# Performance work log

Hardware: AMD Instinct MI355X
Metric: run time of the kernel (lower is better)

## Reference

```python
import jax, jax.numpy as jnp
import numpy as np

D_MODEL = 512
N = 1024
BS = 64


def setup_inputs() -> dict:
    key = jax.random.key(0)
    ks = jax.random.split(key, 4)
    x = jax.random.normal(ks[0], (BS, N, D_MODEL), dtype=jnp.float32)
    # nn.Linear init per init_weights(): weight ~ N(0, 0.001), bias = 0
    Wq = 0.001 * jax.random.normal(ks[1], (D_MODEL, D_MODEL), dtype=jnp.float32)
    Wk = 0.001 * jax.random.normal(ks[2], (D_MODEL, D_MODEL), dtype=jnp.float32)
    Wv = 0.001 * jax.random.normal(ks[3], (D_MODEL, D_MODEL), dtype=jnp.float32)
    bq = jnp.zeros((D_MODEL,), dtype=jnp.float32)
    bk = jnp.zeros((D_MODEL,), dtype=jnp.float32)
    bv = jnp.zeros((D_MODEL,), dtype=jnp.float32)
    pos_bias = jnp.ones((N, N), dtype=jnp.float32)  # nn.Parameter(ones)
    return {"x": x, "Wq": Wq, "bq": bq, "Wk": Wk, "bk": bk,
            "Wv": Wv, "bv": bv, "pos_bias": pos_bias}


def reference(x, Wq, bq, Wk, bk, Wv, bv, pos_bias):
    # q,k,v: [bs, n, d] via Linear (y = x W^T + b)
    q = jnp.einsum('bnd,ed->bne', x, Wq) + bq
    k = jnp.einsum('bnd,ed->bne', x, Wk) + bk
    v = jnp.einsum('bnd,ed->bne', x, Wv) + bv
    # exp(k[b,j,d] + bias[i,j]) factorizes exactly: exp(bias) * exp(k).
    # This avoids the (n, bs, n, d) broadcast intermediate of the original
    # while computing identical math.
    ek = jnp.exp(k)                                   # [bs, n, d]
    eb = jnp.exp(pos_bias)                            # [n_i, n_j]
    numerator = jnp.einsum('ij,bjd->bid', eb, ek * v)  # sum over j
    denominator = jnp.einsum('ij,bjd->bid', eb, ek)
    out = jax.nn.sigmoid(q) * (numerator / denominator)  # [bs, n, d]
    return out
```

## Files before the change

### kernel.cpp

```cpp
#include <hip/hip_runtime.h>
#include <hip/hip_bf16.h>
#include <stdint.h>


#define NSEQ 1024
#define DM   512

typedef __attribute__((ext_vector_type(8))) short bf16x8;
typedef __attribute__((ext_vector_type(4))) float f32x4;

static __device__ __forceinline__ float b2f(unsigned short u) {
    union { uint32_t i; float f; } c; c.i = ((uint32_t)u) << 16; return c.f;
}
static __device__ __forceinline__ unsigned short f2b(float f) {
    union { float f; uint32_t i; } c; c.f = f;
    uint32_t r = c.i + 0x7FFFu + ((c.i >> 16) & 1u);
    return (unsigned short)(r >> 16);
}
static __device__ __forceinline__ void gl_lds16(const unsigned short* g, unsigned short* l) {
    __builtin_amdgcn_global_load_lds(
        (const __attribute__((address_space(1))) unsigned int*)(g),
        (__attribute__((address_space(3))) unsigned int*)(l), 16, 0, 0);
}

#define PH_BAR() do { asm volatile("" ::: "memory"); \
    __builtin_amdgcn_s_barrier(); asm volatile("" ::: "memory"); } while (0)

__global__ void k_flag0(unsigned int* flag) { *flag = 0u; }

__global__ void k_flag(const float* __restrict__ pb, unsigned int* __restrict__ flag) {
    int i = blockIdx.x * 256 + threadIdx.x;
    float4 v = reinterpret_cast<const float4*>(pb)[i];
    float p0 = pb[0];
    if (v.x != p0 || v.y != p0 || v.z != p0 || v.w != p0) atomicOr(flag, 1u);
}

__global__ void k_eb(const float* __restrict__ pb, unsigned short* __restrict__ eb,
                     const unsigned int* __restrict__ flag) {
    if (*flag == 0u) return;
    int i = blockIdx.x * 256 + threadIdx.x;
    float4 v = reinterpret_cast<const float4*>(pb)[i];
    union { unsigned short u[4]; uint2 p; } o;
    o.u[0] = f2b(__expf(v.x)); o.u[1] = f2b(__expf(v.y));
    o.u[2] = f2b(__expf(v.z)); o.u[3] = f2b(__expf(v.w));
    reinterpret_cast<uint2*>(eb)[i] = o.p;
}

__global__ void k_cvt(const float* __restrict__ src, unsigned short* __restrict__ dst) {
    int i = blockIdx.x * 256 + threadIdx.x;
    const float4* p = reinterpret_cast<const float4*>(src) + (size_t)i * 2;
    float4 f0 = p[0], f1 = p[1];
    union { unsigned short u[8]; int4 v; } o;
    o.u[0]=f2b(f0.x); o.u[1]=f2b(f0.y); o.u[2]=f2b(f0.z); o.u[3]=f2b(f0.w);
    o.u[4]=f2b(f1.x); o.u[5]=f2b(f1.y); o.u[6]=f2b(f1.z); o.u[7]=f2b(f1.w);
    reinterpret_cast<int4*>(dst)[i] = o.v;
}

__global__ void k_cvt_kv(const float* __restrict__ src, unsigned short* __restrict__ Wb,
                         int toff) {
    int i = blockIdx.x * 256 + threadIdx.x;
    int r = i >> 6, c8 = i & 63;
    const float4* p = reinterpret_cast<const float4*>(src + (size_t)r * DM + c8 * 8);
    float4 f0 = p[0], f1 = p[1];
    union { unsigned short u[8]; int4 v; } o;
    o.u[0]=f2b(f0.x); o.u[1]=f2b(f0.y); o.u[2]=f2b(f0.z); o.u[3]=f2b(f0.w);
    o.u[4]=f2b(f1.x); o.u[5]=f2b(f1.y); o.u[6]=f2b(f1.z); o.u[7]=f2b(f1.w);
    int r2 = 512 + ((r >> 7) << 8) + ((r & 127) << 1) + toff;
    *reinterpret_cast<int4*>(&Wb[(size_t)r2 * DM + c8 * 8]) = o.v;
}

template<int NT>
static __device__ __forceinline__ void gemm_p(
    const unsigned short* __restrict__ Abase,
    const unsigned short* __restrict__ Bbase,
    int lda, int ldb, unsigned short* smem, f32x4 (&acc)[8][4],
    int wave, int lane)
{
    const int wr = wave >> 2, wq = wave & 3;
    const int lrow = lane & 15, lkg = lane >> 4;
    const int po  = lane >> 3;
    const int sub = (lane >> 2) & 1;
    const int qp  = lane & 3;

    auto stage = [&](int mat, int s, int h, int t) {
        int p = h * 64 + wave * 8 + po;
        int r = p * 2 + sub;
        int q = qp ^ (p & 3);
        int col = ((t & (NT - 1)) << 5) + q * 8;
        const unsigned short* g = (mat ? Bbase + (size_t)r * ldb
                                       : Abase + (size_t)r * lda) + col;
        unsigned short* d = smem + mat * 32768 + s * 8192 + (h * 64 + wave * 8) * 64;
        gl_lds16(g, d);
    };
    auto loadA = [&](int s, int h, bf16x8* af) {
        const unsigned short* base = smem + s * 8192;
        #pragma unroll
        for (int mi = 0; mi < 4; ++mi) {
            int r = wr * 128 + h * 64 + mi * 16 + lrow;
            int p = r >> 1;
            af[mi] = *reinterpret_cast<const bf16x8*>(
                base + p * 64 + (r & 1) * 32 + ((lkg ^ (p & 3)) << 3));
        }
    };
    auto loadB = [&](int s, bf16x8* bf) {
        const unsigned short* base = smem + 32768 + s * 8192;
        #pragma unroll
        for (int ni = 0; ni < 4; ++ni) {
            int r = wq * 64 + ni * 16 + lrow;
            int p = r >> 1;
            bf[ni] = *reinterpret_cast<const bf16x8*>(
                base + p * 64 + (r & 1) * 32 + ((lkg ^ (p & 3)) << 3));
        }
    };
    auto mfma16 = [&](int h, bf16x8* af, bf16x8* bf) {
        __builtin_amdgcn_s_setprio(1);
        #pragma unroll
        for (int mi = 0; mi < 4; ++mi)
            #pragma unroll
            for (int ni = 0; ni < 4; ++ni)
                acc[h * 4 + mi][ni] = __builtin_amdgcn_mfma_f32_16x16x32_bf16(
                    af[mi], bf[ni], acc[h * 4 + mi][ni], 0, 0, 0);
        __builtin_amdgcn_s_setprio(0);
    };

    #pragma unroll
    for (int pt = 0; pt < 3; ++pt) {
        stage(0, pt, 0, pt); stage(0, pt, 1, pt);
        stage(1, pt, 0, pt); stage(1, pt, 1, pt);
    }
    asm volatile("s_waitcnt vmcnt(8)" ::: "memory");
    __builtin_amdgcn_s_barrier();

    #pragma unroll 1
    for (int tt = 0; tt < NT; tt += 4) {
        #pragma unroll
        for (int u = 0; u < 4; ++u) {
            const int t = tt + u;
            const int s = u, s3 = (u + 3) & 3, t3 = t + 3;
            bf16x8 af[4], bfr[4];
            loadB(s, bfr); loadA(s, 0, af);
            stage(0, s3, 0, t3); stage(0, s3, 1, t3);
            mfma16(0, af, bfr);
            loadA(s, 1, af);
            stage(1, s3, 0, t3); stage(1, s3, 1, t3);
            mfma16(1, af, bfr);
            asm volatile("s_waitcnt vmcnt(8)" ::: "memory");
            __builtin_amdgcn_s_barrier();
        }
    }
    asm volatile("s_waitcnt vmcnt(0)" ::: "memory");
    __builtin_amdgcn_s_barrier();
}

__launch_bounds__(512)
__global__ void k_kv(const unsigned short* __restrict__ xb,
                     const unsigned short* __restrict__ Wb,
                     const float* __restrict__ bk, const float* __restrict__ bv,
                     unsigned short* __restrict__ Z,
                     float* __restrict__ P,
                     const unsigned int* __restrict__ flag)
{
    extern __shared__ unsigned short smem[];
    const int bid = blockIdx.x;
    const int logical = (bid & 7) * 128 + (bid >> 3);
    const int mtile = logical >> 2, e4 = logical & 3;
    const int brow = mtile * 256;
    const int b = brow >> 10, jtile = (brow >> 8) & 3;
    const bool uni = (*flag == 0u);

    const int tid = threadIdx.x;
    const int lane = tid & 63, wave = tid >> 6;
    const int wr = wave >> 2, wq = wave & 3;
    const int lrow = lane & 15, lkg = lane >> 4;

    f32x4 acc[8][4];
    const f32x4 z4 = {0.f, 0.f, 0.f, 0.f};
    #pragma unroll
    for (int a = 0; a < 8; ++a)
        #pragma unroll
        for (int c = 0; c < 4; ++c) acc[a][c] = z4;

    gemm_p<16>(xb + (size_t)brow * DM, Wb + (size_t)(512 + e4 * 256) * DM, DM, DM,
               smem, acc, wave, lane);

    if (uni) {
        const int sub = lrow & 1;
        float* SF = reinterpret_cast<float*>(smem);
        float se[4], sv2[4];
        #pragma unroll
        for (int ni = 0; ni < 4; ++ni) {
            int n = wq * 64 + ni * 16 + lrow;
            int d = e4 * 128 + (n >> 1);
            float bia = sub ? bv[d] : bk[d];
            float accv = 0.f, acce = 0.f;
            #pragma unroll
            for (int mi = 0; mi < 8; ++mi) {
                #pragma unroll
                for (int r = 0; r < 4; ++r) {
                    float val = acc[mi][ni][r] + bia;
                    float e = sub ? val : __expf(val);
                    float partner = __shfl_xor(e, 1);
                    if (!sub) { accv += e * partner; acce += e; }
                }
            }
            accv += __shfl_xor(accv, 16); accv += __shfl_xor(accv, 32);
            acce += __shfl_xor(acce, 16); acce += __shfl_xor(acce, 32);
            se[ni] = acce; sv2[ni] = accv;
        }
        __syncthreads();
        if (sub == 0 && lkg == 0) {
            #pragma unroll
            for (int ni = 0; ni < 4; ++ni) {
                int dl = wq * 32 + ni * 8 + (lrow >> 1);
                SF[wr * 256 + dl * 2]     = sv2[ni];
                SF[wr * 256 + dl * 2 + 1] = se[ni];
            }
        }
        __syncthreads();
        if (tid < 128) {
            int dl = tid, d = e4 * 128 + dl;
            float num = SF[dl * 2]     + SF[256 + dl * 2];
            float den = SF[dl * 2 + 1] + SF[256 + dl * 2 + 1];
            P[b * 2048 + jtile * 512 + d] = num;
            P[131072 + b * 2048 + jtile * 512 + d] = den;
        }
    } else {
        unsigned short* T = smem;
        #pragma unroll
        for (int pp = 0; pp < 2; ++pp) {
            __syncthreads();
            if (wr == pp) {
                #pragma unroll
                for (int mi = 0; mi < 8; ++mi) {
                    int m0 = mi*16 + lkg*4;
                    #pragma unroll
                    for (int ni = 0; ni < 4; ++ni) {
                        int n = wq*64 + ni*16 + lrow;
                        int sub = n & 1;
                        int d = e4 * 128 + (n >> 1);
                        float bia = sub ? bv[d] : bk[d];
                        union { unsigned short u[4]; uint2 p; } o;
                        #pragma unroll
                        for (int r = 0; r < 4; ++r) {
                            float tv = acc[mi][ni][r] + bia;
                            o.u[r] = f2b(sub ? tv : __expf(tv));
                        }
                        *reinterpret_cast<uint2*>(&T[n * 136 + m0]) = o.p;
                    }
                }
            }
            __syncthreads();
            const int j0 = (brow & (NSEQ - 1)) + pp * 128;
            #pragma unroll
            for (int it = 0; it < 8; ++it) {
                int idx = it * 512 + tid;
                int zr = idx >> 4, jg = idx & 15;
                int t = zr >> 7, dli = zr & 127;
                int d = e4 * 128 + dli;
                union { unsigned short u[8]; int4 v; } o;
                if (t == 0) {
                    union { unsigned short u[8]; int4 v; } pe, pv;
                    pe.v = *reinterpret_cast<const int4*>(&T[(2*dli)     * 136 + jg*8]);
                    pv.v = *reinterpret_cast<const int4*>(&T[(2*dli + 1) * 136 + jg*8]);
                    #pragma unroll
                    for (int j = 0; j < 8; ++j) o.u[j] = f2b(b2f(pe.u[j]) * b2f(pv.u[j]));
                } else {
                    o.v = *reinterpret_cast<const int4*>(&T[(2*dli) * 136 + jg*8]);
                }
                int nz = ((d >> 4) << 5) + t * 16 + (d & 15);
                size_t off = ((size_t)(b * NSEQ + nz)) * NSEQ + j0 + jg * 8;
                *reinterpret_cast<int4*>(&Z[off]) = o.v;
            }
        }
    }
}

__launch_bounds__(256)
__global__ void k_sum2(const float* __restrict__ P,
                       const unsigned int* __restrict__ flag,
                       float* __restrict__ R)
{
    if (*flag != 0u) return;
    int gid = blockIdx.x * 256 + threadIdx.x;
    int b = gid >> 9, d = gid & 511;
    const float* p0 = P + b * 2048 + d;
    const float* p1 = P + 131072 + b * 2048 + d;
    float num = p0[0] + p0[512] + p0[1024] + p0[1536];
    float den = p1[0] + p1[512] + p1[1024] + p1[1536];
    R[gid] = num / den;
}

__launch_bounds__(512)
__global__ void k_q(const unsigned short* __restrict__ xb,
                    const unsigned short* __restrict__ Wb,
                    const float* __restrict__ bq,
                    const float* __restrict__ R,
                    unsigned short* __restrict__ s_out,
                    float* __restrict__ out,
                    const unsigned int* __restrict__ flag)
{
    extern __shared__ unsigned short smem[];
    const int bid = blockIdx.x;
    const int logical = (bid & 7) * 64 + (bid >> 3);
    const int mtile = logical >> 1, etile = logical & 1;
    const int brow = mtile * 256;
    const int ecol = etile * 256;
    const int b = brow >> 10;
    const bool uni = (*flag == 0u);

    const int tid = threadIdx.x;
    const int lane = tid & 63, wave = tid >> 6;
    const int wr = wave >> 2, wq = wave & 3;
    const int lrow = lane & 15, lkg = lane >> 4;

    f32x4 acc[8][4];
    const f32x4 z4 = {0.f, 0.f, 0.f, 0.f};
    #pragma unroll
    for (int a = 0; a < 8; ++a)
        #pragma unroll
        for (int c = 0; c < 4; ++c) acc[a][c] = z4;

    gemm_p<16>(xb + (size_t)brow * DM, Wb + (size_t)ecol * DM, DM, DM,
               smem, acc, wave, lane);

    unsigned short* T = smem;
    #pragma unroll
    for (int pp = 0; pp < 2; ++pp) {
        __syncthreads();
        if ((wq >> 1) == pp) {
            #pragma unroll
            for (int mi = 0; mi < 8; ++mi) {
                int m0 = wr*128 + mi*16 + lkg*4;
                #pragma unroll
                for (int ni = 0; ni < 4; ++ni) {
                    int nl = (wq & 1) * 64 + ni*16 + lrow;
                    float bia = bq[ecol + pp*128 + nl];
                    #pragma unroll
                    for (int r = 0; r < 4; ++r) {
                        float tq = acc[mi][ni][r] + bia;
                        float sg = __builtin_amdgcn_rcpf(1.f + __expf(-tq));
                        T[(m0 + r) * 136 + nl] = f2b(sg);
                    }
                }
            }
        }
        __syncthreads();
        if (uni) {
            #pragma unroll
            for (int it = 0; it < 8; ++it) {
                int idx = it * 512 + tid;
                int m = idx >> 4, ng = idx & 15;
                union { unsigned short u[8]; int4 v; } sv;
                sv.v = *reinterpret_cast<const int4*>(&T[m * 136 + ng * 8]);
                int dcol = ecol + pp * 128 + ng * 8;
                const float4* rp = reinterpret_cast<const float4*>(&R[b * 512 + dcol]);
                float4 r0 = rp[0], r1 = rp[1];
                float4 o0, o1;
                o0.x = b2f(sv.u[0]) * r0.x; o0.y = b2f(sv.u[1]) * r0.y;
                o0.z = b2f(sv.u[2]) * r0.z; o0.w = b2f(sv.u[3]) * r0.w;
                o1.x = b2f(sv.u[4]) * r1.x; o1.y = b2f(sv.u[5]) * r1.y;
                o1.z = b2f(sv.u[6]) * r1.z; o1.w = b2f(sv.u[7]) * r1.w;
                float4* op = reinterpret_cast<float4*>(
                    &out[(size_t)(brow + m) * DM + dcol]);
                op[0] = o0; op[1] = o1;
            }
        } else {
            #pragma unroll
            for (int it = 0; it < 8; ++it) {
                int idx = it * 512 + tid;
                int m = idx >> 4, ng = idx & 15;
                int4 vv = *reinterpret_cast<const int4*>(&T[m * 136 + ng * 8]);
                *reinterpret_cast<int4*>(
                    &s_out[(size_t)(brow + m) * DM + ecol + pp*128 + ng * 8]) = vv;
            }
        }
    }
}

__launch_bounds__(512)
__global__ void k_aft(const unsigned short* __restrict__ eb,
                      const unsigned short* __restrict__ Z,
                      const unsigned short* __restrict__ s_in,
                      const unsigned int* __restrict__ flag,
                      float* __restrict__ out)
{
    if (*flag == 0u) return;
    extern __shared__ unsigned short smem[];
    const int bid = blockIdx.x;
    const int logical = (bid & 7) * 32 + (bid >> 3);
    const int itile = logical & 3, ncol = logical >> 2;
    const int i0 = itile * 256;

    const int tid = threadIdx.x;
    const int lane = tid & 63, wave = tid >> 6;
    const int wr = wave >> 2, wq = wave & 3;
    const int lrow = lane & 15, lkg = lane >> 4;
    const int po = lane >> 3, sub = (lane >> 2) & 1, qp = lane & 3;
    const int ch0 = wave * 2;

    const unsigned short* Abase = eb + (size_t)i0 * NSEQ;
    const unsigned short* Bbase = Z + (size_t)ncol * 4 * 256 * NSEQ;

    f32x4 acc[8][4];
    const f32x4 z4 = {0.f, 0.f, 0.f, 0.f};
    #pragma unroll
    for (int a = 0; a < 8; ++a)
        #pragma unroll
        for (int c = 0; c < 4; ++c) acc[a][c] = z4;

    auto half = [&](int isB, int d, int c) -> unsigned short* {
        return smem + isB * 32768 + (d * 2 + c) * 8192;
    };
    auto stg = [&](int isB, int d, int c, int t) {
        int ta = t & 63, gp = ta >> 4, tk = ta & 15;
        unsigned short* dst = half(isB, d, c);
        #pragma unroll
        for (int q2 = 0; q2 < 2; ++q2) {
            int ch = ch0 + q2;
            int p = ch * 8 + po, r = p * 2 + sub;
            int col = (tk << 6) + (c << 5) + ((qp ^ (p & 3)) << 3);
            const unsigned short* g = isB
                ? Bbase + ((size_t)(gp * 256 + r)) * NSEQ + col
                : Abase + (size_t)r * NSEQ + col;
            gl_lds16(g, dst + ch * 512);
        }
    };
    auto ldA = [&](int d, int c, int h, bf16x8* af) {
        const unsigned short* base = half(0, d, c);
        #pragma unroll
        for (int mi = 0; mi < 4; ++mi) {
            int r = wr * 128 + h * 64 + mi * 16 + lrow, p = r >> 1;
            af[mi] = *reinterpret_cast<const bf16x8*>(
                base + p * 64 + (r & 1) * 32 + ((lkg ^ (p & 3)) << 3));
        }
    };
    auto ldB = [&](int d, int c, bf16x8* bf) {
        const unsigned short* base = half(1, d, c);
        #pragma unroll
        for (int ni = 0; ni < 4; ++ni) {
            int r = wq * 64 + ni * 16 + lrow, p = r >> 1;
            bf[ni] = *reinterpret_cast<const bf16x8*>(
                base + p * 64 + (r & 1) * 32 + ((lkg ^ (p & 3)) << 3));
        }
    };
    auto mm = [&](int h, bf16x8* af, bf16x8* bf) {
        __builtin_amdgcn_s_setprio(1);
        #pragma unroll
        for (int mi = 0; mi < 4; ++mi)
            #pragma unroll
            for (int ni = 0; ni < 4; ++ni)
                acc[h * 4 + mi][ni] = __builtin_amdgcn_mfma_f32_16x16x32_bf16(
                    af[mi], bf[ni], acc[h * 4 + mi][ni], 0, 0, 0);
        __builtin_amdgcn_s_setprio(0);
    };

    stg(0, 0, 0, 0); stg(1, 0, 0, 0);
    stg(0, 0, 1, 0); stg(1, 0, 1, 0);
    stg(0, 1, 0, 1); stg(1, 1, 0, 1);
    asm volatile("s_waitcnt vmcnt(4)" ::: "memory");
    __builtin_amdgcn_s_barrier();
    asm volatile("" ::: "memory");

    #pragma unroll 1
    for (int g = 0; g < 4; ++g) {
        #pragma unroll 1
        for (int ii = 0; ii < 8; ++ii) {
            const int T = (g << 4) + (ii << 1);
            const int U = T + 1, T2 = T + 2, U2 = T + 3;
            bf16x8 af[4], bf[4];
            ldB(0, 0, bf); ldA(0, 0, 0, af); stg(0, 1, 1, U);
            PH_BAR(); mm(0, af, bf); PH_BAR();
            ldA(0, 0, 1, af); stg(1, 1, 1, U);
            PH_BAR(); mm(1, af, bf); PH_BAR();
            ldB(0, 1, bf); ldA(0, 1, 0, af); stg(0, 0, 0, T2);
            PH_BAR(); mm(0, af, bf); PH_BAR();
            ldA(0, 1, 1, af); stg(1, 0, 0, T2);
            asm volatile("s_waitcnt vmcnt(4)" ::: "memory");
            PH_BAR(); mm(1, af, bf); PH_BAR();
            ldB(1, 0, bf); ldA(1, 0, 0, af); stg(0, 0, 1, T2);
            PH_BAR(); mm(0, af, bf); PH_BAR();
            ldA(1, 0, 1, af); stg(1, 0, 1, T2);
            PH_BAR(); mm(1, af, bf); PH_BAR();
            ldB(1, 1, bf); ldA(1, 1, 0, af); stg(0, 1, 0, U2);
            PH_BAR(); mm(0, af, bf); PH_BAR();
            ldA(1, 1, 1, af); stg(1, 1, 0, U2);
            asm volatile("s_waitcnt vmcnt(4)" ::: "memory");
            PH_BAR(); mm(1, af, bf); PH_BAR();
        }
        const int n0 = (ncol * 4 + g) * 256;
        #pragma unroll
        for (int mi = 0; mi < 8; ++mi) {
            int i = i0 + wr*128 + mi*16 + lkg*4;
            #pragma unroll
            for (int pi = 0; pi < 2; ++pi) {
                int nA = n0 + wq*64 + pi*32 + lrow;
                int b  = nA >> 10, nn = nA & (NSEQ - 1);
                int d  = ((nn >> 5) << 4) + (nn & 15);
                #pragma unroll
                for (int r = 0; r < 4; ++r) {
                    size_t o = ((size_t)(b * NSEQ + i + r)) * DM + d;
                    out[o] = b2f(s_in[o]) * acc[mi][pi*2][r] / acc[mi][pi*2 + 1][r];
                }
                acc[mi][pi*2] = z4; acc[mi][pi*2 + 1] = z4;
            }
        }
    }
    asm volatile("s_waitcnt vmcnt(0)" ::: "memory");
}

extern "C" void kernel_launch(void* const* d_in, const int* in_sizes, int n_in,
                              void* d_out, int out_size, void* d_ws, size_t ws_size,
                              hipStream_t stream)
{
    const float* x  = (const float*)d_in[0];
    const float* Wq = (const float*)d_in[1];
    const float* bq = (const float*)d_in[2];
    const float* Wk = (const float*)d_in[3];
    const float* bk = (const float*)d_in[4];
    const float* Wv = (const float*)d_in[5];
    const float* bv = (const float*)d_in[6];
    const float* pb = (const float*)d_in[7];
    float* out = (float*)d_out;

    char* ws = (char*)d_ws;
    unsigned short* eb   = (unsigned short*)(ws);
    float*          Pbuf = (float*)(ws);
    unsigned short* Wb   = (unsigned short*)(ws + ((size_t)2 << 20));
    unsigned int*   flag = (unsigned int*)(ws + 0x380000);
    float*          Rbuf = (float*)(ws + 0x384000);
    unsigned short* xb   = (unsigned short*)(ws + ((size_t)4   << 20));
    unsigned short* s    = (unsigned short*)(ws + ((size_t)68  << 20));
    unsigned short* Z    = (unsigned short*)(ws + ((size_t)132 << 20));

    k_flag0<<<1, 1, 0, stream>>>(flag);
    k_flag<<<1024, 256, 0, stream>>>(pb, flag);
    k_eb <<<1024, 256, 0, stream>>>(pb, eb, flag);
    k_cvt<<<16384, 256, 0, stream>>>(x,  xb);
    k_cvt<<<128,   256, 0, stream>>>(Wq, Wb);
    k_cvt_kv<<<128, 256, 0, stream>>>(Wk, Wb, 0);
    k_cvt_kv<<<128, 256, 0, stream>>>(Wv, Wb, 1);
    k_kv<<<1024, 512, 131072, stream>>>(xb, Wb, bk, bv, Z, Pbuf, flag);
    k_sum2<<<128, 256, 0, stream>>>(Pbuf, flag, Rbuf);
    k_q<<<512, 512, 131072, stream>>>(xb, Wb, bq, Rbuf, s, out, flag);
    k_aft<<<256, 512, 131072, stream>>>(eb, Z, s, flag, out);
}
```

Before: 212.8 us.

## Shrink k_q tiles to 128x128 with inline double-buffered LDS GEMM loop

Rewrites the Q projection kernel to use 128x128 output tiles instead of 256x256. It replaces the shared gemm_p helper with an inline double-buffered global-to-LDS pipeline using swizzled addressing. Shared memory drops to about 34KB and the grid grows to 2048 blocks, which should raise occupancy and improve load balance across CUs. The cost is less data reuse per block, so more global and L2 traffic is spent on re-reading x and W. It also changes the sub-lane selector in k_kv from lrow&1 to lane&1; since lane&15 and lane keep the same low bit, this is equivalent.

```diff
diff --git a/kernel.cpp b/kernel.cpp
--- a/kernel.cpp
+++ b/kernel.cpp
@@ -184,7 +184,7 @@
                smem, acc, wave, lane);
 
     if (uni) {
-        const int sub = lrow & 1;
+        const int sub = lane & 1;
         float* SF = reinterpret_cast<float*>(smem);
         float se[4], sv2[4];
         #pragma unroll
@@ -301,10 +301,10 @@
 {
     extern __shared__ unsigned short smem[];
     const int bid = blockIdx.x;
-    const int logical = (bid & 7) * 64 + (bid >> 3);
-    const int mtile = logical >> 1, etile = logical & 1;
-    const int brow = mtile * 256;
-    const int ecol = etile * 256;
+    const int logical = (bid & 7) * 256 + (bid >> 3);
+    const int mtile = logical >> 2, etile = logical & 3;
+    const int brow = mtile * 128;
+    const int ecol = etile * 128;
     const int b = brow >> 10;
     const bool uni = (*flag == 0u);
 
@@ -312,67 +312,115 @@
     const int lane = tid & 63, wave = tid >> 6;
     const int wr = wave >> 2, wq = wave & 3;
     const int lrow = lane & 15, lkg = lane >> 4;
-
-    f32x4 acc[8][4];
+    const int po = lane >> 3, sub = (lane >> 2) & 1, qp = lane & 3;
+
+    const unsigned short* Abase = xb + (size_t)brow * DM;
+    const unsigned short* Bbase = Wb + (size_t)ecol * DM;
+
+    f32x4 acc[4][2];
     const f32x4 z4 = {0.f, 0.f, 0.f, 0.f};
     #pragma unroll
-    for (int a = 0; a < 8; ++a)
-        #pragma unroll
-        for (int c = 0; c < 4; ++c) acc[a][c] = z4;
-
-    gemm_p<16>(xb + (size_t)brow * DM, Wb + (size_t)ecol * DM, DM, DM,
-               smem, acc, wave, lane);
+    for (int a = 0; a < 4; ++a)
+        #pragma unroll
+        for (int c = 0; c < 2; ++c) acc[a][c] = z4;
+
+    auto stg = [&](int mat, int s, int t) {
+        int p = wave * 8 + po;
+        int r = p * 2 + sub;
+        int q = qp ^ (p & 3);
+        int col = (t << 5) + q * 8;
+        const unsigned short* g = (mat ? Bbase + (size_t)r * DM
+                                       : Abase + (size_t)r * DM) + col;
+        gl_lds16(g, smem + mat * 8192 + s * 4096 + (wave * 8) * 64);
+    };
+    auto ldA = [&](int s, bf16x8* af) {
+        const unsigned short* base = smem + s * 4096;
+        #pragma unroll
+        for (int mi = 0; mi < 4; ++mi) {
+            int r = wr * 64 + mi * 16 + lrow, p = r >> 1;
+            af[mi] = *reinterpret_cast<const bf16x8*>(
+                base + p * 64 + (r & 1) * 32 + ((lkg ^ (p & 3)) << 3));
+        }
+    };
+    auto ldB = [&](int s, bf16x8* bf) {
+        const unsigned short* base = smem + 8192 + s * 4096;
+        #pragma unroll
+        for (int ni = 0; ni < 2; ++ni) {
+            int r = wq * 32 + ni * 16 + lrow, p = r >> 1;
+            bf[ni] = *reinterpret_cast<const bf16x8*>(
+                base + p * 64 + (r & 1) * 32 + ((lkg ^ (p & 3)) << 3));
+        }
+    };
+
+    stg(0, 0, 0); stg(1, 0, 0);
+    asm volatile("s_waitcnt vmcnt(0)" ::: "memory");
+    __builtin_amdgcn_s_barrier();
+
+    #pragma unroll 1
+    for (int tt = 0; tt < 16; tt += 2) {
+        #pragma unroll
+        for (int u = 0; u < 2; ++u) {
+            const int t = tt + u;
+            const int s = u, sn = u ^ 1;
+            if (t + 1 < 16) { stg(0, sn, t + 1); stg(1, sn, t + 1); }
+            bf16x8 af[4], bf[2];
+            ldB(s, bf); ldA(s, af);
+            __builtin_amdgcn_s_setprio(1);
+            #pragma unroll
+            for (int mi = 0; mi < 4; ++mi)
+                #pragma unroll
+                for (int ni = 0; ni < 2; ++ni)
+                    acc[mi][ni] = __builtin_amdgcn_mfma_f32_16x16x32_bf16(
+                        af[mi], bf[ni], acc[mi][ni], 0, 0, 0);
+            __builtin_amdgcn_s_setprio(0);
+            asm volatile("s_waitcnt vmcnt(0)" ::: "memory");
+            __builtin_amdgcn_s_barrier();
+        }
+    }
 
     unsigned short* T = smem;
     #pragma unroll
-    for (int pp = 0; pp < 2; ++pp) {
-        __syncthreads();
-        if ((wq >> 1) == pp) {
-            #pragma unroll
-            for (int mi = 0; mi < 8; ++mi) {
-                int m0 = wr*128 + mi*16 + lkg*4;
-                #pragma unroll
-                for (int ni = 0; ni < 4; ++ni) {
-                    int nl = (wq & 1) * 64 + ni*16 + lrow;
-                    float bia = bq[ecol + pp*128 + nl];
-                    #pragma unroll
-                    for (int r = 0; r < 4; ++r) {
-                        float tq = acc[mi][ni][r] + bia;
-                        float sg = __builtin_amdgcn_rcpf(1.f + __expf(-tq));
-                        T[(m0 + r) * 136 + nl] = f2b(sg);
-                    }
-                }
+    for (int mi = 0; mi < 4; ++mi) {
+        int m0 = wr * 64 + mi * 16 + lkg * 4;
+        #pragma unroll
+        for (int ni = 0; ni < 2; ++ni) {
+            int nl = wq * 32 + ni * 16 + lrow;
+            float bia = bq[ecol + nl];
+            #pragma unroll
+            for (int r = 0; r < 4; ++r) {
+                float tq = acc[mi][ni][r] + bia;
+                float sg = __builtin_amdgcn_rcpf(1.f + __expf(-tq));
+                T[(m0 + r) * 136 + nl] = f2b(sg);
             }
         }
-        __syncthreads();
-        if (uni) {
-            #pragma unroll
-            for (int it = 0; it < 8; ++it) {
-                int idx = it * 512 + tid;
-                int m = idx >> 4, ng = idx & 15;
-                union { unsigned short u[8]; int4 v; } sv;
-                sv.v = *reinterpret_cast<const int4*>(&T[m * 136 + ng * 8]);
-                int dcol = ecol + pp * 128 + ng * 8;
-                const float4* rp = reinterpret_cast<const float4*>(&R[b * 512 + dcol]);
-                float4 r0 = rp[0], r1 = rp[1];
-                float4 o0, o1;
-                o0.x = b2f(sv.u[0]) * r0.x; o0.y = b2f(sv.u[1]) * r0.y;
-                o0.z = b2f(sv.u[2]) * r0.z; o0.w = b2f(sv.u[3]) * r0.w;
-                o1.x = b2f(sv.u[4]) * r1.x; o1.y = b2f(sv.u[5]) * r1.y;
-                o1.z = b2f(sv.u[6]) * r1.z; o1.w = b2f(sv.u[7]) * r1.w;
-                float4* op = reinterpret_cast<float4*>(
-                    &out[(size_t)(brow + m) * DM + dcol]);
-                op[0] = o0; op[1] = o1;
-            }
-        } else {
-            #pragma unroll
-            for (int it = 0; it < 8; ++it) {
-                int idx = it * 512 + tid;
-                int m = idx >> 4, ng = idx & 15;
-                int4 vv = *reinterpret_cast<const int4*>(&T[m * 136 + ng * 8]);
-                *reinterpret_cast<int4*>(
-                    &s_out[(size_t)(brow + m) * DM + ecol + pp*128 + ng * 8]) = vv;
-            }
+    }
+    __syncthreads();
+    if (uni) {
+        #pragma unroll
+        for (int it = 0; it < 4; ++it) {
+            int idx = it * 512 + tid;
+            int m = idx >> 4, ng = idx & 15;
+            union { unsigned short u[8]; int4 v; } sv;
+            sv.v = *reinterpret_cast<const int4*>(&T[m * 136 + ng * 8]);
+            int dcol = ecol + ng * 8;
+            const float4* rp = reinterpret_cast<const float4*>(&R[b * 512 + dcol]);
+            float4 r0 = rp[0], r1 = rp[1];
+            float4 o0, o1;
+            o0.x = b2f(sv.u[0]) * r0.x; o0.y = b2f(sv.u[1]) * r0.y;
+            o0.z = b2f(sv.u[2]) * r0.z; o0.w = b2f(sv.u[3]) * r0.w;
+            o1.x = b2f(sv.u[4]) * r1.x; o1.y = b2f(sv.u[5]) * r1.y;
+            o1.z = b2f(sv.u[6]) * r1.z; o1.w = b2f(sv.u[7]) * r1.w;
+            float4* op = reinterpret_cast<float4*>(&out[(size_t)(brow + m) * DM + dcol]);
+            op[0] = o0; op[1] = o1;
+        }
+    } else {
+        #pragma unroll
+        for (int it = 0; it < 4; ++it) {
+            int idx = it * 512 + tid;
+            int m = idx >> 4, ng = idx & 15;
+            int4 vv = *reinterpret_cast<const int4*>(&T[m * 136 + ng * 8]);
+            *reinterpret_cast<int4*>(
+                &s_out[(size_t)(brow + m) * DM + ecol + ng * 8]) = vv;
         }
     }
 }
@@ -541,6 +589,6 @@
     k_cvt_kv<<<128, 256, 0, stream>>>(Wv, Wb, 1);
     k_kv<<<1024, 512, 131072, stream>>>(xb, Wb, bk, bv, Z, Pbuf, flag);
     k_sum2<<<128, 256, 0, stream>>>(Pbuf, flag, Rbuf);
-    k_q<<<512, 512, 131072, stream>>>(xb, Wb, bq, Rbuf, s, out, flag);
+    k_q<<<2048, 512, 34816, stream>>>(xb, Wb, bq, Rbuf, s, out, flag);
     k_aft<<<256, 512, 131072, stream>>>(eb, Z, s, flag, out);
 }
```

After: 196.3 us. -7.8%, faster.
